# Kernel optimization log

Hardware: AMD Instinct MI355X
Metric: run time of the kernel (lower is better)

## Reference

```python
import jax, jax.numpy as jnp
import numpy as np

NEG_INF = -1e30  # finite stand-in for -inf masking (avoids NaN rows/grads)


def setup_inputs() -> dict:
    key = jax.random.key(0)
    k1, k2, k3 = jax.random.split(key, 3)
    B, T, D = 4, 2048, 1024
    x = jax.random.normal(k1, (B, T, D), dtype=jnp.float32)
    attention_mask = jnp.ones((B, T), dtype=bool)  # True = valid (non-pad) token
    # nn.Linear weights: out = x @ W.T ; scaled for sane magnitudes
    w_qkv = jax.random.normal(k2, (3 * D, D), dtype=jnp.float32) * (D ** -0.5)
    w_proj = jax.random.normal(k3, (D, D), dtype=jnp.float32) * (D ** -0.5)
    return {"x": x, "attention_mask": attention_mask,
            "w_qkv": w_qkv, "w_proj": w_proj, "n_heads": 16}


def reference(x, attention_mask, w_qkv, w_proj, n_heads):
    B, T, D = x.shape
    H = n_heads
    hd = D // H
    qkv = (x @ w_qkv.T).reshape(B, T, 3, H, hd)
    q, k, v = qkv[:, :, 0], qkv[:, :, 1], qkv[:, :, 2]  # each [B,T,H,hd]
    q = q.transpose(0, 2, 1, 3)  # [B,H,T,hd]
    k = k.transpose(0, 2, 1, 3)
    v = v.transpose(0, 2, 1, 3)

    scale = 1.0 / jnp.sqrt(jnp.asarray(hd, dtype=x.dtype))
    scores = jnp.einsum("bhqd,bhkd->bhqk", q, k) * scale  # [B,H,T,T]

    causal = jnp.tril(jnp.ones((T, T), dtype=bool))            # [T,T]
    valid = causal[None, None, :, :] & attention_mask[:, None, None, :]  # [B,1,T,T] via bcast
    scores = jnp.where(valid, scores, NEG_INF)

    attn = jax.nn.softmax(scores, axis=-1)
    out = jnp.einsum("bhqk,bhkd->bhqd", attn, v)  # [B,H,T,hd]
    out = out.transpose(0, 2, 1, 3).reshape(B, T, D)
    return out @ w_proj.T
```

## Files before the change

kernel.cpp:

```cpp
#include <hip/hip_runtime.h>
#include <stdint.h>

typedef unsigned short u16;
typedef __bf16 bf16x8 __attribute__((ext_vector_type(8)));
typedef __bf16 bf16x4v __attribute__((ext_vector_type(4)));
typedef float f32x4 __attribute__((ext_vector_type(4)));
typedef u16 u16x8 __attribute__((ext_vector_type(8)));

typedef void gv_t __attribute__((address_space(1)));
typedef void lv_t __attribute__((address_space(3)));

__device__ __forceinline__ void glds16(const void* g, const void* l) {
  __builtin_amdgcn_global_load_lds((gv_t*)(uintptr_t)g,
                                   (lv_t*)(unsigned)(uintptr_t)l, 16, 0, 0);
}

__device__ __forceinline__ u16 f2bf(float f) {
  union { float f; unsigned u; } v; v.f = f;
  return (u16)((v.u + 0x7fffu + ((v.u >> 16) & 1u)) >> 16);
}

#define MFMA(a, b, c) __builtin_amdgcn_mfma_f32_16x16x32_bf16(a, b, c, 0, 0, 0)

__global__ __launch_bounds__(256) void cvt4(const float* __restrict__ in,
                                            u16* __restrict__ out, int n4) {
  int i = blockIdx.x * 256 + threadIdx.x;
  if (i >= n4) return;
  float4 f = ((const float4*)in)[i];
  ushort4 r;
  r.x = f2bf(f.x); r.y = f2bf(f.y); r.z = f2bf(f.z); r.w = f2bf(f.w);
  ((ushort4*)out)[i] = r;
}

template <bool F32OUT>
__global__ __launch_bounds__(256) void gemm_bt(const u16* __restrict__ A,
                                               const u16* __restrict__ B,
                                               void* __restrict__ C,
                                               int M, int N, int K) {
  __shared__ u16 As[128 * 32];
  __shared__ u16 Bs[128 * 32];
  const int tid = threadIdx.x;
  const int wid = tid >> 6, lane = tid & 63;
  const int wr = wid >> 1, wc = wid & 1;
  const int g = lane >> 4, c = lane & 15;
  const int nwg = gridDim.x * gridDim.y;
  int bid = blockIdx.y * gridDim.x + blockIdx.x;
  bid = (bid & 7) * (nwg >> 3) + (bid >> 3);
  const int bx = bid % gridDim.x, by = bid / gridDim.x;
  const int m0 = by << 7, n0 = bx << 7;

  const f32x4 fzero = {0.f, 0.f, 0.f, 0.f};
  f32x4 acc[4][4];
#pragma unroll
  for (int i = 0; i < 4; ++i)
#pragma unroll
    for (int j = 0; j < 4; ++j) acc[i][j] = fzero;

  const int srow = lane >> 2;
  const int scol = (lane & 3) * 8;
  const u16* Ab = A + (size_t)m0 * K;
  const u16* Bb = B + (size_t)n0 * K;
  const int nk = K >> 5;
  for (int kt = 0; kt < nk; ++kt) {
    const int k0 = kt << 5;
    glds16(Ab + (size_t)((wid)*16 + srow) * K + k0 + scol, &As[(wid)*512]);
    glds16(Ab + (size_t)((wid + 4) * 16 + srow) * K + k0 + scol, &As[(wid + 4) * 512]);
    glds16(Bb + (size_t)((wid)*16 + srow) * K + k0 + scol, &Bs[(wid)*512]);
    glds16(Bb + (size_t)((wid + 4) * 16 + srow) * K + k0 + scol, &Bs[(wid + 4) * 512]);
    __syncthreads();
    bf16x8 af[4], bfr[4];
#pragma unroll
    for (int i = 0; i < 4; ++i) {
      af[i]  = *(const bf16x8*)&As[(wr * 64 + i * 16 + c) * 32 + g * 8];
      bfr[i] = *(const bf16x8*)&Bs[(wc * 64 + i * 16 + c) * 32 + g * 8];
    }
#pragma unroll
    for (int i = 0; i < 4; ++i)
#pragma unroll
      for (int j = 0; j < 4; ++j) acc[i][j] = MFMA(af[i], bfr[j], acc[i][j]);
    __syncthreads();
  }
#pragma unroll
  for (int i = 0; i < 4; ++i) {
    const int row0 = m0 + wr * 64 + i * 16 + g * 4;
#pragma unroll
    for (int j = 0; j < 4; ++j) {
      const int col = n0 + wc * 64 + j * 16 + c;
#pragma unroll
      for (int r = 0; r < 4; ++r) {
        if (F32OUT)
          ((float*)C)[(size_t)(row0 + r) * N + col] = acc[i][j][r];
        else
          ((u16*)C)[(size_t)(row0 + r) * N + col] = f2bf(acc[i][j][r]);
      }
    }
  }
}

__global__ __launch_bounds__(256, 3) void attn_fwd(const u16* __restrict__ qkv,
                                                   u16* __restrict__ aout) {
  __shared__ u16 Kl[2][4096];
  __shared__ u16 Vl[2][64 * 72];
  __shared__ u16 Plds[4][2][1056];
  const int tid = threadIdx.x;
  const int wid = tid >> 6, lane = tid & 63;
  const int g = lane >> 4, c = lane & 15;
  const int h = blockIdx.y, b = blockIdx.z;

  const f32x4 fzero = {0.f, 0.f, 0.f, 0.f};

  const u16* kbase = qkv + (size_t)(b * 2048) * 3072 + 1024 + h * 64;
  const u16* vbase = kbase + 1024;
  const u16* ksrc = kbase + (size_t)(wid * 16 + (lane >> 3)) * 3072 +
                    ((lane & 7) ^ (lane >> 3)) * 8;
  const int st = tid >> 3;
  const int sd = (tid & 7) * 8;
  const int vswz = (tid & 7) << 3;
  const int kfb = c * 64 + ((g ^ (c & 3)) << 3) + (((c >> 2) & 1) << 5);
  const float C2 = 0.18033688f;

#pragma unroll 1
  for (int pass = 0; pass < 2; ++pass) {
    const int qt = pass ? (15 - blockIdx.x) : blockIdx.x;
    const int qb = qt << 7;
    const int nkt = 2 * qt + 2;
    const int q00 = qb + wid * 32 + g * 4;
    const int qsw = qb + wid * 32 + c;
    const int wqmax = qb + wid * 32 + 31;

    bf16x8 qf[2][2];
    {
      const u16* qp = qkv + (size_t)(b * 2048 + qb + wid * 32 + c) * 3072 +
                      h * 64 + g * 8;
      qf[0][0] = *(const bf16x8*)qp;
      qf[0][1] = *(const bf16x8*)(qp + 32);
      qf[1][0] = *(const bf16x8*)(qp + (size_t)16 * 3072);
      qf[1][1] = *(const bf16x8*)(qp + (size_t)16 * 3072 + 32);
    }

    f32x4 o[2][4];
#pragma unroll
    for (int a = 0; a < 2; ++a)
#pragma unroll
      for (int n = 0; n < 4; ++n) o[a][n] = fzero;
    float m_i[2] = {-1e30f, -1e30f}, l_i[2] = {0.f, 0.f};

    glds16(ksrc, &Kl[0][wid * 1024]);
    glds16(ksrc + (size_t)8 * 3072, &Kl[0][wid * 1024 + 512]);
    {
      const u16* vp = vbase + (size_t)st * 3072 + sd;
      u16x8 v0 = *(const u16x8*)vp;
      u16x8 v1 = *(const u16x8*)(vp + (size_t)32 * 3072);
#pragma unroll
      for (int j = 0; j < 8; ++j) {
        Vl[0][(sd + j) * 72 + (st ^ vswz)] = v0[j];
        Vl[0][(sd + j) * 72 + ((st + 32) ^ vswz)] = v1[j];
      }
    }
    __syncthreads();

    int buf = 0;
    for (int kt = 0; kt < nkt; ++kt) {
      const int nbuf = buf ^ 1;
      const int kb = kt << 6;
      u16x8 vreg0, vreg1;
      const bool pfetch = (kt + 1 < nkt);
      if (pfetch) {
        const size_t toff = (size_t)(kt + 1) * 64 * 3072;
        glds16(ksrc + toff, &Kl[nbuf][wid * 1024]);
        glds16(ksrc + toff + (size_t)8 * 3072, &Kl[nbuf][wid * 1024 + 512]);
        const u16* vp = vbase + toff + (size_t)st * 3072 + sd;
        vreg0 = *(const u16x8*)vp;
        vreg1 = *(const u16x8*)(vp + (size_t)32 * 3072);
      }

      if (kb <= wqmax) {
        const u16* Kb = &Kl[buf][0];
        f32x4 s[2][4];
        __builtin_amdgcn_s_setprio(1);
#pragma unroll
        for (int n = 0; n < 4; ++n) {
          const bf16x8 kf0 = *(const bf16x8*)&Kb[n * 1024 + kfb];
          const bf16x8 kf1 = *(const bf16x8*)&Kb[n * 1024 + (kfb ^ 32)];
#pragma unroll
          for (int a = 0; a < 2; ++a) {
            f32x4 t = MFMA(kf0, qf[a][0], fzero);
            s[a][n] = MFMA(kf1, qf[a][1], t);
          }
        }
        __builtin_amdgcn_s_setprio(0);
        if (kt >= nkt - 2) {
#pragma unroll
          for (int a = 0; a < 2; ++a)
#pragma unroll
            for (int n = 0; n < 4; ++n)
#pragma unroll
              for (int r = 0; r < 4; ++r)
                s[a][n][r] = (kb + n * 16 + 4 * g + r <= qsw + a * 16)
                                 ? s[a][n][r] : -1e30f;
        }
        float fs[2], rs[2];
#pragma unroll
        for (int a = 0; a < 2; ++a) {
          f32x4 mm = s[a][0];
#pragma unroll
          for (int n = 1; n < 4; ++n)
#pragma unroll
            for (int r = 0; r < 4; ++r) mm[r] = fmaxf(mm[r], s[a][n][r]);
          float rm = fmaxf(fmaxf(mm[0], mm[1]), fmaxf(mm[2], mm[3]));
          rm = fmaxf(rm, __shfl_xor(rm, 16));
          rm = fmaxf(rm, __shfl_xor(rm, 32));
          const float mn = fmaxf(m_i[a], rm);
          fs[a] = exp2f((m_i[a] - mn) * C2);
          m_i[a] = mn;
          const float mC = mn * C2;
          float rsl = 0.f;
#pragma unroll
          for (int n = 0; n < 4; ++n) {
            float p0 = exp2f(fmaf(s[a][n][0], C2, -mC));
            float p1 = exp2f(fmaf(s[a][n][1], C2, -mC));
            float p2 = exp2f(fmaf(s[a][n][2], C2, -mC));
            float p3 = exp2f(fmaf(s[a][n][3], C2, -mC));
            rsl += (p0 + p1) + (p2 + p3);
            bf16x4v pw = {(__bf16)p0, (__bf16)p1, (__bf16)p2, (__bf16)p3};
            *(bf16x4v*)&Plds[wid][a][c * 66 + 16 * n + 4 * g] = pw;
          }
          rsl += __shfl_xor(rsl, 16);
          rsl += __shfl_xor(rsl, 32);
          rs[a] = rsl;
          l_i[a] = l_i[a] * fs[a] + rs[a];
        }
        float fso[2][4];
#pragma unroll
        for (int a = 0; a < 2; ++a)
#pragma unroll
          for (int r = 0; r < 4; ++r) fso[a][r] = __shfl(fs[a], 4 * g + r);
#pragma unroll
        for (int a = 0; a < 2; ++a)
#pragma unroll
          for (int n = 0; n < 4; ++n)
#pragma unroll
            for (int r = 0; r < 4; ++r) o[a][n][r] *= fso[a][r];
        bf16x8 pf0[2], pf1[2];
#pragma unroll
        for (int a = 0; a < 2; ++a) {
          pf0[a] = *(const bf16x8*)&Plds[wid][a][c * 66 + g * 8];
          pf1[a] = *(const bf16x8*)&Plds[wid][a][c * 66 + 32 + g * 8];
        }
        const u16* Vb = &Vl[buf][0];
        __builtin_amdgcn_s_setprio(1);
#pragma unroll
        for (int n = 0; n < 4; ++n) {
          const int f = (2 * n + (c >> 3)) & 7;
          const bf16x8 vf0 =
              *(const bf16x8*)&Vb[(n * 16 + c) * 72 + 8 * (g ^ f)];
          const bf16x8 vf1 =
              *(const bf16x8*)&Vb[(n * 16 + c) * 72 + 8 * ((4 + g) ^ f)];
#pragma unroll
          for (int a = 0; a < 2; ++a) {
            o[a][n] = MFMA(pf0[a], vf0, o[a][n]);
            o[a][n] = MFMA(pf1[a], vf1, o[a][n]);
          }
        }
        __builtin_amdgcn_s_setprio(0);
      }

      if (pfetch) {
#pragma unroll
        for (int j = 0; j < 8; ++j) {
          Vl[nbuf][(sd + j) * 72 + (st ^ vswz)] = vreg0[j];
          Vl[nbuf][(sd + j) * 72 + ((st + 32) ^ vswz)] = vreg1[j];
        }
      }
      __syncthreads();
      buf = nbuf;
    }

#pragma unroll
    for (int a = 0; a < 2; ++a) {
      const float inv = 1.0f / l_i[a];
      float invo[4];
#pragma unroll
      for (int r = 0; r < 4; ++r) invo[r] = __shfl(inv, 4 * g + r);
      u16* op = aout + (size_t)(b * 2048 + q00 + a * 16) * 1024 + h * 64;
#pragma unroll
      for (int n = 0; n < 4; ++n)
#pragma unroll
        for (int r = 0; r < 4; ++r)
          op[(size_t)r * 1024 + n * 16 + c] = f2bf(o[a][n][r] * invo[r]);
    }
  }
}

extern "C" void kernel_launch(void* const* d_in, const int* in_sizes, int n_in,
                              void* d_out, int out_size, void* d_ws, size_t ws_size,
                              hipStream_t stream) {
  const float* x = (const float*)d_in[0];
  const float* wqkv = (const float*)d_in[2];
  const float* wproj = (const float*)d_in[3];
  float* out = (float*)d_out;

  u16* ws = (u16*)d_ws;
  u16* xb     = ws;
  u16* wqkvb  = xb + 8388608;
  u16* wprojb = wqkvb + 3145728;
  u16* qkvb   = wprojb + 1048576;
  u16* aob    = qkvb + 25165824;

  cvt4<<<8192, 256, 0, stream>>>(x, xb, 2097152);
  cvt4<<<3072, 256, 0, stream>>>(wqkv, wqkvb, 786432);
  cvt4<<<1024, 256, 0, stream>>>(wproj, wprojb, 262144);

  gemm_bt<false><<<dim3(24, 64), 256, 0, stream>>>(xb, wqkvb, (void*)qkvb,
                                                   8192, 3072, 1024);
  attn_fwd<<<dim3(8, 16, 4), 256, 0, stream>>>(qkvb, aob);
  gemm_bt<true><<<dim3(8, 64), 256, 0, stream>>>(aob, wprojb, (void*)out,
                                                 8192, 1024, 1024);
}
```

Baseline: 213.8 us.

## Split attention block across 8 waves with 16 query rows each

The attention kernel now launches 512 threads per block, with each of 8 waves owning 16 query rows instead of 4 waves owning 32. K/V tile loading is spread over twice as many threads, so each thread issues one load instead of two. The causal mask is applied only on the single diagonal tile per wave. This aims for more parallelism and latency hiding and fewer registers per wave, at the cost of each wave reusing every K/V LDS fragment for half as many query rows and more block-wide barrier participants.

```diff
diff --git a/kernel.cpp b/kernel.cpp
--- a/kernel.cpp
+++ b/kernel.cpp
@@ -97,11 +97,11 @@
   }
 }
 
-__global__ __launch_bounds__(256, 3) void attn_fwd(const u16* __restrict__ qkv,
+__global__ __launch_bounds__(512, 4) void attn_fwd(const u16* __restrict__ qkv,
                                                    u16* __restrict__ aout) {
   __shared__ u16 Kl[2][4096];
   __shared__ u16 Vl[2][64 * 72];
-  __shared__ u16 Plds[4][2][1056];
+  __shared__ u16 Plds[8][1056];
   const int tid = threadIdx.x;
   const int wid = tid >> 6, lane = tid & 63;
   const int g = lane >> 4, c = lane & 15;
@@ -111,7 +111,7 @@
 
   const u16* kbase = qkv + (size_t)(b * 2048) * 3072 + 1024 + h * 64;
   const u16* vbase = kbase + 1024;
-  const u16* ksrc = kbase + (size_t)(wid * 16 + (lane >> 3)) * 3072 +
+  const u16* ksrc = kbase + (size_t)(wid * 8 + (lane >> 3)) * 3072 +
                     ((lane & 7) ^ (lane >> 3)) * 8;
   const int st = tid >> 3;
   const int sd = (tid & 7) * 8;
@@ -124,38 +124,30 @@
     const int qt = pass ? (15 - blockIdx.x) : blockIdx.x;
     const int qb = qt << 7;
     const int nkt = 2 * qt + 2;
-    const int q00 = qb + wid * 32 + g * 4;
-    const int qsw = qb + wid * 32 + c;
-    const int wqmax = qb + wid * 32 + 31;
-
-    bf16x8 qf[2][2];
+    const int q00 = qb + wid * 16 + g * 4;
+    const int qsw = qb + wid * 16 + c;
+    const int wqmax = qb + wid * 16 + 15;
+    const int ktmask = wqmax >> 6;
+
+    bf16x8 qf0, qf1;
     {
-      const u16* qp = qkv + (size_t)(b * 2048 + qb + wid * 32 + c) * 3072 +
+      const u16* qp = qkv + (size_t)(b * 2048 + qb + wid * 16 + c) * 3072 +
                       h * 64 + g * 8;
-      qf[0][0] = *(const bf16x8*)qp;
-      qf[0][1] = *(const bf16x8*)(qp + 32);
-      qf[1][0] = *(const bf16x8*)(qp + (size_t)16 * 3072);
-      qf[1][1] = *(const bf16x8*)(qp + (size_t)16 * 3072 + 32);
-    }
-
-    f32x4 o[2][4];
-#pragma unroll
-    for (int a = 0; a < 2; ++a)
-#pragma unroll
-      for (int n = 0; n < 4; ++n) o[a][n] = fzero;
-    float m_i[2] = {-1e30f, -1e30f}, l_i[2] = {0.f, 0.f};
-
-    glds16(ksrc, &Kl[0][wid * 1024]);
-    glds16(ksrc + (size_t)8 * 3072, &Kl[0][wid * 1024 + 512]);
+      qf0 = *(const bf16x8*)qp;
+      qf1 = *(const bf16x8*)(qp + 32);
+    }
+
+    f32x4 o[4];
+#pragma unroll
+    for (int n = 0; n < 4; ++n) o[n] = fzero;
+    float m_i = -1e30f, l_i = 0.f;
+
+    glds16(ksrc, &Kl[0][wid * 512]);
     {
-      const u16* vp = vbase + (size_t)st * 3072 + sd;
-      u16x8 v0 = *(const u16x8*)vp;
-      u16x8 v1 = *(const u16x8*)(vp + (size_t)32 * 3072);
-#pragma unroll
-      for (int j = 0; j < 8; ++j) {
+      u16x8 v0 = *(const u16x8*)(vbase + (size_t)st * 3072 + sd);
+#pragma unroll
+      for (int j = 0; j < 8; ++j)
         Vl[0][(sd + j) * 72 + (st ^ vswz)] = v0[j];
-        Vl[0][(sd + j) * 72 + ((st + 32) ^ vswz)] = v1[j];
-      }
     }
     __syncthreads();
 
@@ -163,90 +155,68 @@
     for (int kt = 0; kt < nkt; ++kt) {
       const int nbuf = buf ^ 1;
       const int kb = kt << 6;
-      u16x8 vreg0, vreg1;
+      u16x8 vreg;
       const bool pfetch = (kt + 1 < nkt);
       if (pfetch) {
         const size_t toff = (size_t)(kt + 1) * 64 * 3072;
-        glds16(ksrc + toff, &Kl[nbuf][wid * 1024]);
-        glds16(ksrc + toff + (size_t)8 * 3072, &Kl[nbuf][wid * 1024 + 512]);
-        const u16* vp = vbase + toff + (size_t)st * 3072 + sd;
-        vreg0 = *(const u16x8*)vp;
-        vreg1 = *(const u16x8*)(vp + (size_t)32 * 3072);
+        glds16(ksrc + toff, &Kl[nbuf][wid * 512]);
+        vreg = *(const u16x8*)(vbase + toff + (size_t)st * 3072 + sd);
       }
 
       if (kb <= wqmax) {
         const u16* Kb = &Kl[buf][0];
-        f32x4 s[2][4];
+        f32x4 s[4];
         __builtin_amdgcn_s_setprio(1);
 #pragma unroll
         for (int n = 0; n < 4; ++n) {
           const bf16x8 kf0 = *(const bf16x8*)&Kb[n * 1024 + kfb];
           const bf16x8 kf1 = *(const bf16x8*)&Kb[n * 1024 + (kfb ^ 32)];
-#pragma unroll
-          for (int a = 0; a < 2; ++a) {
-            f32x4 t = MFMA(kf0, qf[a][0], fzero);
-            s[a][n] = MFMA(kf1, qf[a][1], t);
-          }
+          f32x4 t = MFMA(kf0, qf0, fzero);
+          s[n] = MFMA(kf1, qf1, t);
         }
         __builtin_amdgcn_s_setprio(0);
-        if (kt >= nkt - 2) {
-#pragma unroll
-          for (int a = 0; a < 2; ++a)
-#pragma unroll
-            for (int n = 0; n < 4; ++n)
-#pragma unroll
-              for (int r = 0; r < 4; ++r)
-                s[a][n][r] = (kb + n * 16 + 4 * g + r <= qsw + a * 16)
-                                 ? s[a][n][r] : -1e30f;
-        }
-        float fs[2], rs[2];
-#pragma unroll
-        for (int a = 0; a < 2; ++a) {
-          f32x4 mm = s[a][0];
-#pragma unroll
-          for (int n = 1; n < 4; ++n)
-#pragma unroll
-            for (int r = 0; r < 4; ++r) mm[r] = fmaxf(mm[r], s[a][n][r]);
-          float rm = fmaxf(fmaxf(mm[0], mm[1]), fmaxf(mm[2], mm[3]));
-          rm = fmaxf(rm, __shfl_xor(rm, 16));
-          rm = fmaxf(rm, __shfl_xor(rm, 32));
-          const float mn = fmaxf(m_i[a], rm);
-          fs[a] = exp2f((m_i[a] - mn) * C2);
-          m_i[a] = mn;
-          const float mC = mn * C2;
-          float rsl = 0.f;
-#pragma unroll
-          for (int n = 0; n < 4; ++n) {
-            float p0 = exp2f(fmaf(s[a][n][0], C2, -mC));
-            float p1 = exp2f(fmaf(s[a][n][1], C2, -mC));
-            float p2 = exp2f(fmaf(s[a][n][2], C2, -mC));
-            float p3 = exp2f(fmaf(s[a][n][3], C2, -mC));
-            rsl += (p0 + p1) + (p2 + p3);
-            bf16x4v pw = {(__bf16)p0, (__bf16)p1, (__bf16)p2, (__bf16)p3};
-            *(bf16x4v*)&Plds[wid][a][c * 66 + 16 * n + 4 * g] = pw;
-          }
-          rsl += __shfl_xor(rsl, 16);
-          rsl += __shfl_xor(rsl, 32);
-          rs[a] = rsl;
-          l_i[a] = l_i[a] * fs[a] + rs[a];
-        }
-        float fso[2][4];
-#pragma unroll
-        for (int a = 0; a < 2; ++a)
-#pragma unroll
-          for (int r = 0; r < 4; ++r) fso[a][r] = __shfl(fs[a], 4 * g + r);
-#pragma unroll
-        for (int a = 0; a < 2; ++a)
+        if (kt == ktmask) {
 #pragma unroll
           for (int n = 0; n < 4; ++n)
 #pragma unroll
-            for (int r = 0; r < 4; ++r) o[a][n][r] *= fso[a][r];
-        bf16x8 pf0[2], pf1[2];
-#pragma unroll
-        for (int a = 0; a < 2; ++a) {
-          pf0[a] = *(const bf16x8*)&Plds[wid][a][c * 66 + g * 8];
-          pf1[a] = *(const bf16x8*)&Plds[wid][a][c * 66 + 32 + g * 8];
-        }
+            for (int r = 0; r < 4; ++r)
+              s[n][r] = (kb + n * 16 + 4 * g + r <= qsw) ? s[n][r] : -1e30f;
+        }
+        f32x4 mm = s[0];
+#pragma unroll
+        for (int n = 1; n < 4; ++n)
+#pragma unroll
+          for (int r = 0; r < 4; ++r) mm[r] = fmaxf(mm[r], s[n][r]);
+        float rm = fmaxf(fmaxf(mm[0], mm[1]), fmaxf(mm[2], mm[3]));
+        rm = fmaxf(rm, __shfl_xor(rm, 16));
+        rm = fmaxf(rm, __shfl_xor(rm, 32));
+        const float mn = fmaxf(m_i, rm);
+        const float fs = exp2f((m_i - mn) * C2);
+        m_i = mn;
+        const float mC = mn * C2;
+        float rsl = 0.f;
+#pragma unroll
+        for (int n = 0; n < 4; ++n) {
+          float p0 = exp2f(fmaf(s[n][0], C2, -mC));
+          float p1 = exp2f(fmaf(s[n][1], C2, -mC));
+          float p2 = exp2f(fmaf(s[n][2], C2, -mC));
+          float p3 = exp2f(fmaf(s[n][3], C2, -mC));
+          rsl += (p0 + p1) + (p2 + p3);
+          bf16x4v pw = {(__bf16)p0, (__bf16)p1, (__bf16)p2, (__bf16)p3};
+          *(bf16x4v*)&Plds[wid][c * 66 + 16 * n + 4 * g] = pw;
+        }
+        rsl += __shfl_xor(rsl, 16);
+        rsl += __shfl_xor(rsl, 32);
+        l_i = l_i * fs + rsl;
+        float fso[4];
+#pragma unroll
+        for (int r = 0; r < 4; ++r) fso[r] = __shfl(fs, 4 * g + r);
+#pragma unroll
+        for (int n = 0; n < 4; ++n)
+#pragma unroll
+          for (int r = 0; r < 4; ++r) o[n][r] *= fso[r];
+        const bf16x8 pf0 = *(const bf16x8*)&Plds[wid][c * 66 + g * 8];
+        const bf16x8 pf1 = *(const bf16x8*)&Plds[wid][c * 66 + 32 + g * 8];
         const u16* Vb = &Vl[buf][0];
         __builtin_amdgcn_s_setprio(1);
 #pragma unroll
@@ -256,39 +226,31 @@
               *(const bf16x8*)&Vb[(n * 16 + c) * 72 + 8 * (g ^ f)];
           const bf16x8 vf1 =
               *(const bf16x8*)&Vb[(n * 16 + c) * 72 + 8 * ((4 + g) ^ f)];
-#pragma unroll
-          for (int a = 0; a < 2; ++a) {
-            o[a][n] = MFMA(pf0[a], vf0, o[a][n]);
-            o[a][n] = MFMA(pf1[a], vf1, o[a][n]);
-          }
+          o[n] = MFMA(pf0, vf0, o[n]);
+          o[n] = MFMA(pf1, vf1, o[n]);
         }
         __builtin_amdgcn_s_setprio(0);
       }
 
       if (pfetch) {
 #pragma unroll
-        for (int j = 0; j < 8; ++j) {
-          Vl[nbuf][(sd + j) * 72 + (st ^ vswz)] = vreg0[j];
-          Vl[nbuf][(sd + j) * 72 + ((st + 32) ^ vswz)] = vreg1[j];
-        }
+        for (int j = 0; j < 8; ++j)
+          Vl[nbuf][(sd + j) * 72 + (st ^ vswz)] = vreg[j];
       }
       __syncthreads();
       buf = nbuf;
     }
 
-#pragma unroll
-    for (int a = 0; a < 2; ++a) {
-      const float inv = 1.0f / l_i[a];
-      float invo[4];
-#pragma unroll
-      for (int r = 0; r < 4; ++r) invo[r] = __shfl(inv, 4 * g + r);
-      u16* op = aout + (size_t)(b * 2048 + q00 + a * 16) * 1024 + h * 64;
-#pragma unroll
-      for (int n = 0; n < 4; ++n)
-#pragma unroll
-        for (int r = 0; r < 4; ++r)
-          op[(size_t)r * 1024 + n * 16 + c] = f2bf(o[a][n][r] * invo[r]);
-    }
+    const float inv = 1.0f / l_i;
+    float invo[4];
+#pragma unroll
+    for (int r = 0; r < 4; ++r) invo[r] = __shfl(inv, 4 * g + r);
+    u16* op = aout + (size_t)(b * 2048 + q00) * 1024 + h * 64;
+#pragma unroll
+    for (int n = 0; n < 4; ++n)
+#pragma unroll
+      for (int r = 0; r < 4; ++r)
+        op[(size_t)r * 1024 + n * 16 + c] = f2bf(o[n][r] * invo[r]);
   }
 }
 
@@ -313,7 +275,7 @@
 
   gemm_bt<false><<<dim3(24, 64), 256, 0, stream>>>(xb, wqkvb, (void*)qkvb,
                                                    8192, 3072, 1024);
-  attn_fwd<<<dim3(8, 16, 4), 256, 0, stream>>>(qkvb, aob);
+  attn_fwd<<<dim3(8, 16, 4), 512, 0, stream>>>(qkvb, aob);
   gemm_bt<true><<<dim3(8, 64), 256, 0, stream>>>(aob, wprojb, (void*)out,
                                                  8192, 1024, 1024);
 }
```

Result: faster. 202.3 us (-5.4%).
